# Kernel tuning notes

Hardware: AMD Instinct MI355X
Metric: run time of the kernel (lower is better)

Reference implementation:

```python
import jax, jax.numpy as jnp
import numpy as np

TOKENS_PER_LAYER = 16  # v in rearrange 'b l (a v) -> b l a v'


def setup_inputs() -> dict:
    key = jax.random.key(0)
    k1, k2 = jax.random.split(key)
    vocab, embed_dim = 1024, 256
    x = jax.random.normal(k1, (64, 32, embed_dim * TOKENS_PER_LAYER), dtype=jnp.float32)
    # nn.Embedding init: uniform(-1/vocab, 1/vocab)
    emb_weight = jax.random.uniform(k2, (vocab, embed_dim), dtype=jnp.float32,
                                    minval=-1.0 / vocab, maxval=1.0 / vocab)
    return {"x": x, "emb_weight": emb_weight}


def reference(x, emb_weight):
    v = TOKENS_PER_LAYER
    b, l, av = x.shape
    a = av // v  # embed_dim
    # rearrange 'b l (a v) -> b l a v'
    z = x.reshape(b, l, a, v)
    # rearrange 'b l a v -> (b l v) a'
    z_flat = z.transpose(0, 1, 3, 2).reshape(b * l * v, a)
    # pairwise squared L2 distance via sum-of-squares + GEMM: [N, vocab]
    dist = (jnp.sum(z_flat * z_flat, axis=1, keepdims=True)
            + jnp.sum(emb_weight * emb_weight, axis=1)
            - 2.0 * (z_flat @ emb_weight.T))
    tokens = jnp.argmin(dist, axis=-1)  # [N] int
    # embedding gather, then rearrange '(b l v) e -> b l e v'
    z_q = emb_weight[tokens].reshape(b, l, v, a).transpose(0, 1, 3, 2)
    # straight-through decoder input: z + sg(z_q - z)
    decoder_input = z + jax.lax.stop_gradient(z_q - z)
    tokens = tokens.reshape(b, l, v)
    return z_q, decoder_input, tokens
```

## Files before the change

### kernel.cpp

```cpp
#include <hip/hip_runtime.h>


#define A_DIM 256
#define VOCAB 1024
#define NROWS 32768
#define ZQ_ELEMS ((size_t)8388608)
#define TAU_C 3.0e-4f
#define TAU_F 2.0e-4f

typedef _Float16 f16x8 __attribute__((ext_vector_type(8)));
typedef float f32x4 __attribute__((ext_vector_type(4)));

#define WS_EHT   ((size_t)0)
#define WS_ZH    ((size_t)524288)
#define WS_ESQ   ((size_t)17301504)
#define WS_ZSQ   ((size_t)17305600)
#define WS_HALF  ((size_t)17436672)
#define WS_TOK   ((size_t)19009536)
#define WS_PLIST ((size_t)19140608)
#define WS_FLIST ((size_t)19664896)
#define WS_CNT   ((size_t)19795968)
#define WS_NEED  ((size_t)19796096)


__global__ __launch_bounds__(256) void prep_e_kernel(const float* __restrict__ emb,
                                                     float* __restrict__ esq,
                                                     _Float16* __restrict__ eht,
                                                     int* __restrict__ cnt) {
    int j = blockIdx.x * 256 + threadIdx.x;
    if (blockIdx.x == 0 && threadIdx.x < 2) cnt[threadIdx.x] = 0;
    if (j >= VOCAB) return;
    const float4* row = (const float4*)(emb + (size_t)j * A_DIM);
    double s = 0.0;
    #pragma unroll 4
    for (int t = 0; t < A_DIM / 4; ++t) {
        float4 f = row[t];
        float sx = f.x * f.x, sy = f.y * f.y, sz = f.z * f.z, sw = f.w * f.w;
        s += (double)sx + (double)sy + (double)sz + (double)sw;
    }
    esq[j] = (float)s;
    #pragma unroll 4
    for (int kb = 0; kb < 32; ++kb) {
        float4 e0 = row[kb * 2], e1 = row[kb * 2 + 1];
        f16x8 h;
        h[0] = (_Float16)e0.x; h[1] = (_Float16)e0.y; h[2] = (_Float16)e0.z; h[3] = (_Float16)e0.w;
        h[4] = (_Float16)e1.x; h[5] = (_Float16)e1.y; h[6] = (_Float16)e1.z; h[7] = (_Float16)e1.w;
        *(f16x8*)(eht + ((size_t)kb * 1024 + j) * 8) = h;
    }
}

__global__ __launch_bounds__(256) void prep_z_kernel(const float* __restrict__ x,
                                                     _Float16* __restrict__ zh,
                                                     float* __restrict__ zsq) {
    __shared__ float raw[A_DIM * 17];
    const int tid = threadIdx.x;
    const int bl = blockIdx.x;
    #pragma unroll
    for (int t = 0; t < 16; ++t) {
        int f = tid + t * 256;
        raw[(f >> 4) * 17 + (f & 15)] = x[(size_t)bl * 4096 + f];
    }
    __syncthreads();
    #pragma unroll
    for (int t = 0; t < 16; ++t) {
        int f = tid + t * 256;
        int v = f >> 8, a = f & 255;
        zh[((size_t)bl * 16 + v) * 256 + a] = (_Float16)raw[a * 17 + v];
    }
    if (tid < 16) {
        double s = 0.0;
        for (int a = 0; a < A_DIM; ++a) {
            float zf = raw[a * 17 + tid];
            float z2 = zf * zf;
            s += (double)z2;
        }
        zsq[bl * 16 + tid] = (float)s;
    }
}

__global__ __launch_bounds__(256, 2) void mfma_kernel(const _Float16* __restrict__ zh,
                                                      const _Float16* __restrict__ eht,
                                                      const float* __restrict__ esq_g,
                                                      float* __restrict__ halfres) {
    __shared__ __align__(16) _Float16 lb[32 * 64 * 8];
    const int tid = threadIdx.x;
    const int w = tid >> 6;
    const int lane = tid & 63;
    const int q = lane >> 4;
    const int ln = lane & 15;
    const int blk = blockIdx.x;
    const int rowblk = blk >> 1;
    const int half = blk & 1;
    const int row0 = rowblk * 128 + w * 32;

    f16x8 afr[2][8];
    #pragma unroll
    for (int mt = 0; mt < 2; ++mt)
        #pragma unroll
        for (int kt = 0; kt < 8; ++kt)
            afr[mt][kt] = *(const f16x8*)(zh + (size_t)(row0 + mt * 16 + ln) * 256 + kt * 32 + q * 8);

    float tv1[8], tv2[8], tv3[8];
    int   ti1[8], ti2[8], ti3[8];
    #pragma unroll
    for (int s = 0; s < 8; ++s) {
        tv1[s] = 3.0e38f; tv2[s] = 3.0e38f; tv3[s] = 3.0e38f;
        ti1[s] = 0; ti2[s] = 0; ti3[s] = 0;
    }

    for (int chunk = 0; chunk < 8; ++chunk) {
        const int c0 = half * 512 + chunk * 64;
        __syncthreads();
        #pragma unroll
        for (int t = 0; t < 8; ++t) {
            int f = tid + t * 256;
            int kb = f >> 6, c = f & 63;
            *(f16x8*)&lb[((size_t)kb * 64 + c) * 8] =
                *(const f16x8*)(eht + ((size_t)kb * 1024 + c0 + c) * 8);
        }
        __syncthreads();

        f32x4 acc[2][4];
        #pragma unroll
        for (int mt = 0; mt < 2; ++mt)
            #pragma unroll
            for (int nt = 0; nt < 4; ++nt)
                acc[mt][nt] = (f32x4){0.f, 0.f, 0.f, 0.f};

        #pragma unroll
        for (int kt = 0; kt < 8; ++kt) {
            #pragma unroll
            for (int nt = 0; nt < 4; ++nt) {
                f16x8 bfr = *(const f16x8*)&lb[(((size_t)kt * 4 + q) * 64 + nt * 16 + ln) * 8];
                acc[0][nt] = __builtin_amdgcn_mfma_f32_16x16x32_f16(afr[0][kt], bfr, acc[0][nt], 0, 0, 0);
                acc[1][nt] = __builtin_amdgcn_mfma_f32_16x16x32_f16(afr[1][kt], bfr, acc[1][nt], 0, 0, 0);
            }
        }

        #pragma unroll
        for (int nt = 0; nt < 4; ++nt) {
            int c = c0 + nt * 16 + ln;
            float es = esq_g[c];
            #pragma unroll
            for (int mt = 0; mt < 2; ++mt) {
                #pragma unroll
                for (int reg = 0; reg < 4; ++reg) {
                    float s = fmaf(-2.0f, acc[mt][nt][reg], es);
                    int slot = mt * 4 + reg;
                    if (s < tv3[slot]) {
                        if (s < tv2[slot]) {
                            tv3[slot] = tv2[slot]; ti3[slot] = ti2[slot];
                            if (s < tv1[slot]) {
                                tv2[slot] = tv1[slot]; ti2[slot] = ti1[slot];
                                tv1[slot] = s; ti1[slot] = c;
                            } else { tv2[slot] = s; ti2[slot] = c; }
                        } else { tv3[slot] = s; ti3[slot] = c; }
                    }
                }
            }
        }
    }

    #pragma unroll
    for (int slot = 0; slot < 8; ++slot) {
        float v1 = tv1[slot], v2 = tv2[slot], v3 = tv3[slot];
        int i1 = ti1[slot], i2 = ti2[slot], i3 = ti3[slot];
        #pragma unroll
        for (int m = 1; m <= 8; m <<= 1) {
            float ov1 = __shfl_xor(v1, m); int oi1 = __shfl_xor(i1, m);
            float ov2 = __shfl_xor(v2, m); int oi2 = __shfl_xor(i2, m);
            float ov3 = __shfl_xor(v3, m); int oi3 = __shfl_xor(i3, m);
            #define INS3(ov, oi)                                                         \
                if (ov < v3 || (ov == v3 && oi < i3)) {                                  \
                    if (ov < v2 || (ov == v2 && oi < i2)) {                              \
                        v3 = v2; i3 = i2;                                                \
                        if (ov < v1 || (ov == v1 && oi < i1)) {                          \
                            v2 = v1; i2 = i1; v1 = ov; i1 = oi;                          \
                        } else { v2 = ov; i2 = oi; }                                     \
                    } else { v3 = ov; i3 = oi; }                                         \
                }
            INS3(ov1, oi1)
            INS3(ov2, oi2)
            INS3(ov3, oi3)
            #undef INS3
        }
        if (ln == 0) {
            int row = row0 + (slot >> 2) * 16 + q * 4 + (slot & 3);
            float* hp = halfres + ((size_t)row * 2 + half) * 6;
            hp[0] = v1; hp[1] = __int_as_float(i1);
            hp[2] = v2; hp[3] = __int_as_float(i2);
            hp[4] = v3; hp[5] = __int_as_float(i3);
        }
    }
}

__global__ __launch_bounds__(256) void finalize_kernel(const float* __restrict__ halfres,
                                                       int* __restrict__ tok,
                                                       int4* __restrict__ plist,
                                                       int* __restrict__ flist,
                                                       int* __restrict__ cnt,
                                                       float* __restrict__ out) {
    int row = blockIdx.x * 256 + threadIdx.x;
    const float* h0 = halfres + (size_t)row * 12;
    float v1 = h0[0]; int i1 = __float_as_int(h0[1]);
    float v2 = h0[2]; int i2 = __float_as_int(h0[3]);
    float v3 = h0[4]; int i3 = __float_as_int(h0[5]);
    #pragma unroll
    for (int e = 0; e < 3; ++e) {
        float ov = h0[6 + 2 * e]; int oi = __float_as_int(h0[7 + 2 * e]);
        if (ov < v3 || (ov == v3 && oi < i3)) {
            if (ov < v2 || (ov == v2 && oi < i2)) {
                v3 = v2; i3 = i2;
                if (ov < v1 || (ov == v1 && oi < i1)) {
                    v2 = v1; i2 = i1; v1 = ov; i1 = oi;
                } else { v2 = ov; i2 = oi; }
            } else { v3 = ov; i3 = oi; }
        }
    }
    tok[row] = i1;
    out[2 * ZQ_ELEMS + (size_t)row] = (float)i1;
    if (v2 - v1 <= TAU_C) {
        if (v3 - v1 > TAU_C) {
            int p = atomicAdd(&cnt[0], 1);
            plist[p] = make_int4(row, i1, i2, 0);
        } else {
            int p = atomicAdd(&cnt[1], 1);
            flist[p] = row;
        }
    }
}

__global__ __launch_bounds__(256) void rescan2_kernel(const float* __restrict__ x,
                                                      const float* __restrict__ emb,
                                                      const float* __restrict__ esq,
                                                      const float* __restrict__ zsq,
                                                      int* __restrict__ tok,
                                                      const int4* __restrict__ plist,
                                                      const int* __restrict__ flist,
                                                      const int* __restrict__ cnt,
                                                      float* __restrict__ out) {
    __shared__ float zrow[A_DIM];
    __shared__ float wv[4];
    __shared__ int   wi[4];
    const int tid = threadIdx.x;
    const int w = tid >> 6, lane = tid & 63;

    {
        const int nw = gridDim.x * 4;
        const int gw = blockIdx.x * 4 + w;
        const int np = cnt[0];
        for (int i = gw; i < np; i += nw) {
            int4 e = plist[i];
            const int r = e.x, c1 = e.y, c2 = e.z;
            const float* xr = x + (size_t)(r >> 4) * 4096 + (r & 15);
            const float* e1 = emb + (size_t)c1 * A_DIM;
            const float* e2 = emb + (size_t)c2 * A_DIM;
            double d1 = 0.0, d2 = 0.0;
            #pragma unroll
            for (int k = 0; k < 4; ++k) {
                int a = lane + k * 64;
                double zv = (double)xr[a * 16];
                d1 = fma(zv, (double)e1[a], d1);
                d2 = fma(zv, (double)e2[a], d2);
            }
            #pragma unroll
            for (int m = 1; m < 64; m <<= 1) {
                d1 += __shfl_xor(d1, m);
                d2 += __shfl_xor(d2, m);
            }
            if (lane == 0) {
                float zq = zsq[r];
                float A1 = zq + esq[c1];
                float D1 = (float)(2.0 * d1);
                float s1 = A1 - D1;
                float A2 = zq + esq[c2];
                float D2 = (float)(2.0 * d2);
                float s2 = A2 - D2;
                int bi = (s2 < s1 || (s2 == s1 && c2 < c1)) ? c2 : c1;
                tok[r] = bi;
                out[2 * ZQ_ELEMS + (size_t)r] = (float)bi;
            }
        }
    }

    const int nf = cnt[1];
    for (int i = blockIdx.x; i < nf; i += gridDim.x) {
        const int r = flist[i];
        __syncthreads();
        zrow[tid] = x[(size_t)(r >> 4) * 4096 + (size_t)tid * 16 + (r & 15)];
        __syncthreads();

        const float4* e0 = (const float4*)(emb + (size_t)tid * 4 * A_DIM);
        double d0 = 0.0, d1 = 0.0, d2 = 0.0, d3 = 0.0;
        #pragma unroll 8
        for (int k4 = 0; k4 < A_DIM / 4; ++k4) {
            float4 zf = *(const float4*)&zrow[k4 * 4];
            double z0 = (double)zf.x, z1 = (double)zf.y;
            double z2 = (double)zf.z, z3 = (double)zf.w;
            float4 f0 = e0[k4];
            float4 f1 = e0[64 + k4];
            float4 f2 = e0[128 + k4];
            float4 f3 = e0[192 + k4];
            d0 = fma((double)f0.x, z0, d0); d0 = fma((double)f0.y, z1, d0);
            d0 = fma((double)f0.z, z2, d0); d0 = fma((double)f0.w, z3, d0);
            d1 = fma((double)f1.x, z0, d1); d1 = fma((double)f1.y, z1, d1);
            d1 = fma((double)f1.z, z2, d1); d1 = fma((double)f1.w, z3, d1);
            d2 = fma((double)f2.x, z0, d2); d2 = fma((double)f2.y, z1, d2);
            d2 = fma((double)f2.z, z2, d2); d2 = fma((double)f2.w, z3, d2);
            d3 = fma((double)f3.x, z0, d3); d3 = fma((double)f3.y, z1, d3);
            d3 = fma((double)f3.z, z2, d3); d3 = fma((double)f3.w, z3, d3);
        }
        const float zq = zsq[r];
        float bv = 3.0e38f; int bi = 0;
        double dd[4] = {d0, d1, d2, d3};
        #pragma unroll
        for (int cc = 0; cc < 4; ++cc) {
            int c = tid * 4 + cc;
            float A = zq + esq[c];
            float D = (float)(2.0 * dd[cc]);
            float s = A - D;
            if (s < bv) { bv = s; bi = c; }
        }
        #pragma unroll
        for (int m = 1; m < 64; m <<= 1) {
            float ov = __shfl_xor(bv, m); int oi = __shfl_xor(bi, m);
            if (ov < bv || (ov == bv && oi < bi)) { bv = ov; bi = oi; }
        }
        if (lane == 0) { wv[w] = bv; wi[w] = bi; }
        __syncthreads();
        if (tid == 0) {
            float BV = wv[0]; int BI = wi[0];
            #pragma unroll
            for (int t = 1; t < 4; ++t)
                if (wv[t] < BV || (wv[t] == BV && wi[t] < BI)) { BV = wv[t]; BI = wi[t]; }
            tok[r] = BI;
            out[2 * ZQ_ELEMS + (size_t)r] = (float)BI;
        }
    }
}

__global__ __launch_bounds__(256) void gather_kernel(const float* __restrict__ emb,
                                                     const int* __restrict__ tok,
                                                     float* __restrict__ out) {
    __shared__ int t16[16];
    const int tid = threadIdx.x;
    const int bl = blockIdx.x;
    if (tid < 16) t16[tid] = tok[bl * 16 + tid];
    __syncthreads();
    const int a = tid;
    __align__(16) float h[16];
    #pragma unroll
    for (int v = 0; v < 16; ++v) h[v] = emb[(size_t)t16[v] * A_DIM + a];
    size_t base = ((size_t)bl * A_DIM + a) * 16;
    float4* p0 = (float4*)(out + base);
    float4* p1 = (float4*)(out + ZQ_ELEMS + base);
    #pragma unroll
    for (int qq = 0; qq < 4; ++qq) {
        float4 val = *(float4*)&h[qq * 4];
        p0[qq] = val;
        p1[qq] = val;
    }
}


__global__ __launch_bounds__(256) void prep_f(const float* __restrict__ emb,
                                              float* __restrict__ e_sq32) {
    int j = blockIdx.x * 256 + threadIdx.x;
    if (j < VOCAB) {
        const float4* row = (const float4*)(emb + (size_t)j * A_DIM);
        double s = 0.0;
        #pragma unroll 4
        for (int t = 0; t < A_DIM / 4; ++t) {
            float4 f = row[t];
            float sx = f.x * f.x, sy = f.y * f.y, sz = f.z * f.z, sw = f.w * f.w;
            s += (double)sx + (double)sy + (double)sz + (double)sw;
        }
        e_sq32[j] = (float)s;
    }
}

#define FBM 64
#define FBN 256
#define FBK 32
struct SmemF {
    union {
        struct { float zs[FBK][FBM]; float es[FBK][FBN]; };
        float4 mbuf[FBM][32];
        struct { double zrow[A_DIM]; float rbest[256]; int ridx[256]; };
    };
    double zsqp_s[4][FBM];
    float  zsq[FBM];
    int    tok[FBM];
    int    flagrows[FBM];
    int    nflag;
};

__global__ __launch_bounds__(256, 2) void main_f(const float* __restrict__ x,
                                                 const float* __restrict__ emb,
                                                 const float* __restrict__ e_sq32,
                                                 float* __restrict__ out) {
    __shared__ SmemF sm;
    const int tid = threadIdx.x;
    const int tx = tid & 31;
    const int ty = tid >> 5;
    const int blk = blockIdx.x;
    const int row0 = blk * FBM;
    const int bl0 = row0 >> 4;
    const int zrow_id = tid & 63;
    const int zq4     = tid >> 6;

    if (tid == 0) sm.nflag = 0;
    float v1[8], v2[8];
    int   i1[8], i2[8];
    #pragma unroll
    for (int r = 0; r < 8; ++r) { v1[r] = 3.0e38f; v2[r] = 3.0e38f; i1[r] = 0; i2[r] = 0; }
    double zsqp = 0.0;
    float4 zpf[2];
    float4 epf[8];
    for (int ct = 0; ct < VOCAB / FBN; ++ct) {
        float acc[8][8];
        #pragma unroll
        for (int rr = 0; rr < 8; ++rr)
            #pragma unroll
            for (int cc = 0; cc < 8; ++cc) acc[rr][cc] = 0.0f;
        for (int kt = 0; kt < A_DIM / FBK; ++kt) {
            if (kt == 0) {
                #pragma unroll
                for (int t = 0; t < 2; ++t) {
                    int f = tid + t * 256;
                    int v4 = f & 3, g = (f >> 2) & 3, kk = f >> 4;
                    zpf[t] = *(const float4*)(x + (size_t)(bl0 + g) * 4096 + (kt * FBK + kk) * 16 + v4 * 4);
                }
                #pragma unroll
                for (int t = 0; t < 8; ++t) {
                    int f = tid + t * 256;
                    int c = f & 255, k4 = f >> 8;
                    epf[t] = *(const float4*)(emb + (size_t)(ct * FBN + c) * A_DIM + kt * FBK + k4 * 4);
                }
            }
            __syncthreads();
            #pragma unroll
            for (int t = 0; t < 2; ++t) {
                int f = tid + t * 256;
                int v4 = f & 3, g = (f >> 2) & 3, kk = f >> 4;
                *(float4*)&sm.zs[kk][g * 16 + v4 * 4] = zpf[t];
            }
            #pragma unroll
            for (int t = 0; t < 8; ++t) {
                int f = tid + t * 256;
                int c = f & 255, k4 = f >> 8;
                sm.es[k4 * 4 + 0][c] = epf[t].x;
                sm.es[k4 * 4 + 1][c] = epf[t].y;
                sm.es[k4 * 4 + 2][c] = epf[t].z;
                sm.es[k4 * 4 + 3][c] = epf[t].w;
            }
            __syncthreads();
            if (kt + 1 < A_DIM / FBK) {
                #pragma unroll
                for (int t = 0; t < 2; ++t) {
                    int f = tid + t * 256;
                    int v4 = f & 3, g = (f >> 2) & 3, kk = f >> 4;
                    zpf[t] = *(const float4*)(x + (size_t)(bl0 + g) * 4096 + ((kt + 1) * FBK + kk) * 16 + v4 * 4);
                }
                #pragma unroll
                for (int t = 0; t < 8; ++t) {
                    int f = tid + t * 256;
                    int c = f & 255, k4 = f >> 8;
                    epf[t] = *(const float4*)(emb + (size_t)(ct * FBN + c) * A_DIM + (kt + 1) * FBK + k4 * 4);
                }
            }
            if (ct == 0 && (kt >> 1) == zq4) {
                #pragma unroll
                for (int kk = 0; kk < FBK; ++kk) {
                    float zf = sm.zs[kk][zrow_id];
                    float zf2 = zf * zf;
                    zsqp += (double)zf2;
                }
            }
            #pragma unroll 2
            for (int kk = 0; kk < FBK; ++kk) {
                float4 za = *(float4*)&sm.zs[kk][ty * 4];
                float4 zb = *(float4*)&sm.zs[kk][32 + ty * 4];
                float4 ea = *(float4*)&sm.es[kk][tx * 4];
                float4 eb = *(float4*)&sm.es[kk][128 + tx * 4];
                float zv[8] = {za.x, za.y, za.z, za.w, zb.x, zb.y, zb.z, zb.w};
                float ev[8] = {ea.x, ea.y, ea.z, ea.w, eb.x, eb.y, eb.z, eb.w};
                #pragma unroll
                for (int rr = 0; rr < 8; ++rr)
                    #pragma unroll
                    for (int cc = 0; cc < 8; ++cc)
                        acc[rr][cc] = fmaf(zv[rr], ev[cc], acc[rr][cc]);
            }
        }
        if (ct == 0) {
            sm.zsqp_s[zq4][zrow_id] = zsqp;
            __syncthreads();
            if (tid < FBM)
                sm.zsq[tid] = (float)(sm.zsqp_s[0][tid] + sm.zsqp_s[1][tid]
                                    + sm.zsqp_s[2][tid] + sm.zsqp_s[3][tid]);
            __syncthreads();
        }
        float esqv[8];
        #pragma unroll
        for (int cc = 0; cc < 8; ++cc) {
            int c = ct * FBN + (cc >> 2) * 128 + tx * 4 + (cc & 3);
            esqv[cc] = e_sq32[c];
        }
        #pragma unroll
        for (int rr = 0; rr < 8; ++rr) {
            int R = (rr >> 2) * 32 + ty * 4 + (rr & 3);
            float zq = sm.zsq[R];
            #pragma unroll
            for (int cc = 0; cc < 8; ++cc) {
                int c = ct * FBN + (cc >> 2) * 128 + tx * 4 + (cc & 3);
                float A = zq + esqv[cc];
                float s = fmaf(-2.0f, acc[rr][cc], A);
                if (s < v1[rr]) { v2[rr] = v1[rr]; i2[rr] = i1[rr]; v1[rr] = s; i1[rr] = c; }
                else if (s < v2[rr]) { v2[rr] = s; i2[rr] = c; }
            }
        }
    }
    __syncthreads();
    #pragma unroll
    for (int rr = 0; rr < 8; ++rr) {
        int r = (rr >> 2) * 32 + ty * 4 + (rr & 3);
        float4 m;
        m.x = v1[rr]; m.y = __int_as_float(i1[rr]);
        m.z = v2[rr]; m.w = __int_as_float(i2[rr]);
        sm.mbuf[r][tx] = m;
    }
    __syncthreads();
    if (tid < FBM) {
        int r = tid;
        float V1 = 3.0e38f, V2 = 3.0e38f;
        int I1 = 0, I2 = 0;
        for (int t = 0; t < 32; ++t) {
            float4 m = sm.mbuf[r][t];
            float a1 = m.x; int a1i = __float_as_int(m.y);
            float a2 = m.z; int a2i = __float_as_int(m.w);
            if (a1 < V1 || (a1 == V1 && a1i < I1)) { V2 = V1; I2 = I1; V1 = a1; I1 = a1i; }
            else if (a1 < V2 || (a1 == V2 && a1i < I2)) { V2 = a1; I2 = a1i; }
            if (a2 < V1 || (a2 == V1 && a2i < I1)) { V2 = V1; I2 = I1; V1 = a2; I1 = a2i; }
            else if (a2 < V2 || (a2 == V2 && a2i < I2)) { V2 = a2; I2 = a2i; }
        }
        sm.tok[r] = I1;
        if (V2 - V1 <= TAU_F) {
            int pos = atomicAdd(&sm.nflag, 1);
            sm.flagrows[pos] = r;
        }
    }
    __syncthreads();
    const int nf = sm.nflag;
    for (int i = 0; i < nf; ++i) {
        const int rl = sm.flagrows[i];
        const int bl = bl0 + (rl >> 4);
        const int v  = rl & 15;
        const float zqrow = sm.zsq[rl];
        sm.zrow[tid] = (double)x[(size_t)bl * 4096 + (size_t)tid * 16 + v];
        __syncthreads();
        float bv = 3.0e38f; int bi = 0;
        #pragma unroll
        for (int cc = 0; cc < 4; ++cc) {
            int c = tid * 4 + cc;
            const float4* er = (const float4*)(emb + (size_t)c * A_DIM);
            double dot = 0.0;
            #pragma unroll 8
            for (int k4 = 0; k4 < A_DIM / 4; ++k4) {
                float4 f = er[k4];
                dot = fma((double)f.x, sm.zrow[k4 * 4 + 0], dot);
                dot = fma((double)f.y, sm.zrow[k4 * 4 + 1], dot);
                dot = fma((double)f.z, sm.zrow[k4 * 4 + 2], dot);
                dot = fma((double)f.w, sm.zrow[k4 * 4 + 3], dot);
            }
            float A = zqrow + e_sq32[c];
            float D = (float)(2.0 * dot);
            float s = A - D;
            if (s < bv) { bv = s; bi = c; }
        }
        sm.rbest[tid] = bv; sm.ridx[tid] = bi;
        __syncthreads();
        if (tid == 0) {
            float BV = sm.rbest[0]; int BI = sm.ridx[0];
            for (int t = 1; t < 256; ++t) {
                float vv = sm.rbest[t];
                if (vv < BV) { BV = vv; BI = sm.ridx[t]; }
            }
            sm.tok[rl] = BI;
        }
        __syncthreads();
    }
    if (tid < FBM) {
        out[2 * ZQ_ELEMS + (size_t)(row0 + tid)] = (float)sm.tok[tid];
    }
    __syncthreads();
    const int a = tid;
    for (int g = 0; g < 4; ++g) {
        __align__(16) float h[16];
        #pragma unroll
        for (int v = 0; v < 16; ++v) {
            h[v] = emb[(size_t)sm.tok[g * 16 + v] * A_DIM + a];
        }
        size_t base = ((size_t)(bl0 + g) * A_DIM + a) * 16;
        float4* p0 = (float4*)(out + base);
        float4* p1 = (float4*)(out + ZQ_ELEMS + base);
        #pragma unroll
        for (int qq = 0; qq < 4; ++qq) {
            float4 val = *(float4*)&h[qq * 4];
            p0[qq] = val;
            p1[qq] = val;
        }
    }
}

extern "C" void kernel_launch(void* const* d_in, const int* in_sizes, int n_in,
                              void* d_out, int out_size, void* d_ws, size_t ws_size,
                              hipStream_t stream) {
    (void)in_sizes; (void)n_in; (void)out_size;
    const float* x   = (const float*)d_in[0];
    const float* emb = (const float*)d_in[1];
    float* out = (float*)d_out;
    char* ws = (char*)d_ws;

    if (ws_size >= WS_NEED) {
        _Float16* eht = (_Float16*)(ws + WS_EHT);
        _Float16* zh  = (_Float16*)(ws + WS_ZH);
        float* esq    = (float*)(ws + WS_ESQ);
        float* zsq    = (float*)(ws + WS_ZSQ);
        float* half_  = (float*)(ws + WS_HALF);
        int* tok      = (int*)(ws + WS_TOK);
        int4* plist   = (int4*)(ws + WS_PLIST);
        int* flist    = (int*)(ws + WS_FLIST);
        int* cnt      = (int*)(ws + WS_CNT);

        prep_e_kernel<<<4, 256, 0, stream>>>(emb, esq, eht, cnt);
        prep_z_kernel<<<2048, 256, 0, stream>>>(x, zh, zsq);
        mfma_kernel<<<512, 256, 0, stream>>>(zh, eht, esq, half_);
        finalize_kernel<<<128, 256, 0, stream>>>(half_, tok, plist, flist, cnt, out);
        rescan2_kernel<<<256, 256, 0, stream>>>(x, emb, esq, zsq, tok, plist, flist, cnt, out);
        gather_kernel<<<2048, 256, 0, stream>>>(emb, tok, out);
    } else {
        float* e_sq32 = (float*)ws;
        prep_f<<<4, 256, 0, stream>>>(emb, e_sq32);
        main_f<<<512, 256, 0, stream>>>(x, emb, e_sq32, out);
    }
}
```

Measured before the change: 279.0 us.

## Split vocab into quarters with double-buffered async LDS loads in MFMA kernel

```diff
diff --git a/kernel.cpp b/kernel.cpp
--- a/kernel.cpp
+++ b/kernel.cpp
@@ -15,12 +15,18 @@
 #define WS_ZH    ((size_t)524288)
 #define WS_ESQ   ((size_t)17301504)
 #define WS_ZSQ   ((size_t)17305600)
-#define WS_HALF  ((size_t)17436672)
-#define WS_TOK   ((size_t)19009536)
-#define WS_PLIST ((size_t)19140608)
-#define WS_FLIST ((size_t)19664896)
-#define WS_CNT   ((size_t)19795968)
-#define WS_NEED  ((size_t)19796096)
+#define WS_QRES  ((size_t)17436672)
+#define WS_TOK   ((size_t)20582400)
+#define WS_PLIST ((size_t)20713472)
+#define WS_FLIST ((size_t)21237760)
+#define WS_CNT   ((size_t)21368832)
+#define WS_NEED  ((size_t)21368960)
+
+__device__ __forceinline__ void async_copy16(const void* g, void* l) {
+    __builtin_amdgcn_global_load_lds(
+        (const __attribute__((address_space(1))) unsigned int*)g,
+        (__attribute__((address_space(3))) unsigned int*)l, 16, 0, 0);
+}
 
 
 __global__ __launch_bounds__(256) void prep_e_kernel(const float* __restrict__ emb,
@@ -56,9 +62,14 @@
     const int tid = threadIdx.x;
     const int bl = blockIdx.x;
     #pragma unroll
-    for (int t = 0; t < 16; ++t) {
-        int f = tid + t * 256;
-        raw[(f >> 4) * 17 + (f & 15)] = x[(size_t)bl * 4096 + f];
+    for (int t = 0; t < 4; ++t) {
+        int f4 = tid * 4 + t * 1024;
+        float4 val = *(const float4*)(x + (size_t)bl * 4096 + f4);
+        int a = f4 >> 4, v0 = f4 & 15;
+        raw[a * 17 + v0 + 0] = val.x;
+        raw[a * 17 + v0 + 1] = val.y;
+        raw[a * 17 + v0 + 2] = val.z;
+        raw[a * 17 + v0 + 3] = val.w;
     }
     __syncthreads();
     #pragma unroll
@@ -78,20 +89,33 @@
     }
 }
 
-__global__ __launch_bounds__(256, 2) void mfma_kernel(const _Float16* __restrict__ zh,
+__global__ __launch_bounds__(256, 4) void mfma_kernel(const _Float16* __restrict__ zh,
                                                       const _Float16* __restrict__ eht,
                                                       const float* __restrict__ esq_g,
-                                                      float* __restrict__ halfres) {
-    __shared__ __align__(16) _Float16 lb[32 * 64 * 8];
+                                                      float* __restrict__ qres) {
+    __shared__ __align__(16) _Float16 lb[2][32 * 32 * 8];
     const int tid = threadIdx.x;
     const int w = tid >> 6;
     const int lane = tid & 63;
     const int q = lane >> 4;
     const int ln = lane & 15;
-    const int blk = blockIdx.x;
-    const int rowblk = blk >> 1;
-    const int half = blk & 1;
+
+    const int wg = blockIdx.x;
+    const int j = wg >> 3;
+    const int rowblk = (wg & 7) * 32 + (j >> 2);
+    const int quarter = j & 3;
     const int row0 = rowblk * 128 + w * 32;
+    const int cq0 = quarter * 256;
+
+    {
+        #pragma unroll
+        for (int t = 0; t < 4; ++t) {
+            int f = tid + t * 256;
+            const _Float16* gsrc = eht + ((size_t)(f >> 5) * 1024 + cq0 + (f & 31)) * 8;
+            _Float16* ldst = &lb[0][(size_t)(t * 256 + w * 64) * 8];
+            async_copy16(gsrc, ldst);
+        }
+    }
 
     f16x8 afr[2][8];
     #pragma unroll
@@ -109,37 +133,40 @@
     }
 
     for (int chunk = 0; chunk < 8; ++chunk) {
-        const int c0 = half * 512 + chunk * 64;
+        const int b = chunk & 1;
+        asm volatile("s_waitcnt vmcnt(0)" ::: "memory");
         __syncthreads();
-        #pragma unroll
-        for (int t = 0; t < 8; ++t) {
-            int f = tid + t * 256;
-            int kb = f >> 6, c = f & 63;
-            *(f16x8*)&lb[((size_t)kb * 64 + c) * 8] =
-                *(const f16x8*)(eht + ((size_t)kb * 1024 + c0 + c) * 8);
-        }
-        __syncthreads();
-
-        f32x4 acc[2][4];
+        if (chunk + 1 < 8) {
+            const int cb = cq0 + (chunk + 1) * 32;
+            #pragma unroll
+            for (int t = 0; t < 4; ++t) {
+                int f = tid + t * 256;
+                const _Float16* gsrc = eht + ((size_t)(f >> 5) * 1024 + cb + (f & 31)) * 8;
+                _Float16* ldst = &lb[b ^ 1][(size_t)(t * 256 + w * 64) * 8];
+                async_copy16(gsrc, ldst);
+            }
+        }
+
+        f32x4 acc[2][2];
         #pragma unroll
         for (int mt = 0; mt < 2; ++mt)
             #pragma unroll
-            for (int nt = 0; nt < 4; ++nt)
+            for (int nt = 0; nt < 2; ++nt)
                 acc[mt][nt] = (f32x4){0.f, 0.f, 0.f, 0.f};
 
         #pragma unroll
         for (int kt = 0; kt < 8; ++kt) {
             #pragma unroll
-            for (int nt = 0; nt < 4; ++nt) {
-                f16x8 bfr = *(const f16x8*)&lb[(((size_t)kt * 4 + q) * 64 + nt * 16 + ln) * 8];
+            for (int nt = 0; nt < 2; ++nt) {
+                f16x8 bfr = *(const f16x8*)&lb[b][((size_t)(kt * 4 + q) * 32 + nt * 16 + ln) * 8];
                 acc[0][nt] = __builtin_amdgcn_mfma_f32_16x16x32_f16(afr[0][kt], bfr, acc[0][nt], 0, 0, 0);
                 acc[1][nt] = __builtin_amdgcn_mfma_f32_16x16x32_f16(afr[1][kt], bfr, acc[1][nt], 0, 0, 0);
             }
         }
 
         #pragma unroll
-        for (int nt = 0; nt < 4; ++nt) {
-            int c = c0 + nt * 16 + ln;
+        for (int nt = 0; nt < 2; ++nt) {
+            int c = cq0 + chunk * 32 + nt * 16 + ln;
             float es = esq_g[c];
             #pragma unroll
             for (int mt = 0; mt < 2; ++mt) {
@@ -186,7 +213,7 @@
         }
         if (ln == 0) {
             int row = row0 + (slot >> 2) * 16 + q * 4 + (slot & 3);
-            float* hp = halfres + ((size_t)row * 2 + half) * 6;
+            float* hp = qres + ((size_t)row * 4 + quarter) * 6;
             hp[0] = v1; hp[1] = __int_as_float(i1);
             hp[2] = v2; hp[3] = __int_as_float(i2);
             hp[4] = v3; hp[5] = __int_as_float(i3);
@@ -194,19 +221,19 @@
     }
 }
 
-__global__ __launch_bounds__(256) void finalize_kernel(const float* __restrict__ halfres,
+__global__ __launch_bounds__(256) void finalize_kernel(const float* __restrict__ qres,
                                                        int* __restrict__ tok,
                                                        int4* __restrict__ plist,
                                                        int* __restrict__ flist,
                                                        int* __restrict__ cnt,
                                                        float* __restrict__ out) {
     int row = blockIdx.x * 256 + threadIdx.x;
-    const float* h0 = halfres + (size_t)row * 12;
+    const float* h0 = qres + (size_t)row * 24;
     float v1 = h0[0]; int i1 = __float_as_int(h0[1]);
     float v2 = h0[2]; int i2 = __float_as_int(h0[3]);
     float v3 = h0[4]; int i3 = __float_as_int(h0[5]);
     #pragma unroll
-    for (int e = 0; e < 3; ++e) {
+    for (int e = 0; e < 9; ++e) {
         float ov = h0[6 + 2 * e]; int oi = __float_as_int(h0[7 + 2 * e]);
         if (ov < v3 || (ov == v3 && oi < i3)) {
             if (ov < v2 || (ov == v2 && oi < i2)) {
@@ -626,7 +653,7 @@
         _Float16* zh  = (_Float16*)(ws + WS_ZH);
         float* esq    = (float*)(ws + WS_ESQ);
         float* zsq    = (float*)(ws + WS_ZSQ);
-        float* half_  = (float*)(ws + WS_HALF);
+        float* qres   = (float*)(ws + WS_QRES);
         int* tok      = (int*)(ws + WS_TOK);
         int4* plist   = (int4*)(ws + WS_PLIST);
         int* flist    = (int*)(ws + WS_FLIST);
@@ -634,8 +661,8 @@
 
         prep_e_kernel<<<4, 256, 0, stream>>>(emb, esq, eht, cnt);
         prep_z_kernel<<<2048, 256, 0, stream>>>(x, zh, zsq);
-        mfma_kernel<<<512, 256, 0, stream>>>(zh, eht, esq, half_);
-        finalize_kernel<<<128, 256, 0, stream>>>(half_, tok, plist, flist, cnt, out);
+        mfma_kernel<<<1024, 256, 0, stream>>>(zh, eht, esq, qres);
+        finalize_kernel<<<128, 256, 0, stream>>>(qres, tok, plist, flist, cnt, out);
         rescan2_kernel<<<256, 256, 0, stream>>>(x, emb, esq, zsq, tok, plist, flist, cnt, out);
         gather_kernel<<<2048, 256, 0, stream>>>(emb, tok, out);
     } else {
```

Result: slower. 539.2 us (+93.3%).
